# Performance work log

Hardware: AMD Instinct MI355X
Metric: run time of the kernel (lower is better)

## Reference

```python
import jax, jax.numpy as jnp
import numpy as np

N_NODES = 100000
N_EDGES = 3200000
N_FEAT = 256
N_CLASS = 4


def setup_inputs() -> dict:
    key = jax.random.key(0)
    ks = jax.random.split(key, 8)
    x = jax.random.normal(ks[0], (N_NODES, N_FEAT), dtype=jnp.float32)
    edge_index = jax.random.randint(ks[1], (2, N_EDGES), 0, N_NODES, dtype=jnp.int64)
    def xavier(k, shape):
        fan_in, fan_out = shape
        std = np.sqrt(2.0 / (fan_in + fan_out))
        return jax.random.normal(k, shape, dtype=jnp.float32) * std
    return {
        'x': x,
        'edge_index': edge_index,
        'W_gcn': xavier(ks[2], (N_FEAT, 64)),
        'b_gcn': jnp.zeros((64,), jnp.float32),
        'W1': xavier(ks[3], (64, 32)),
        'b1': jnp.zeros((32,), jnp.float32),
        'W2': xavier(ks[4], (32, 16)),
        'b2': jnp.zeros((16,), jnp.float32),
        'W3': xavier(ks[5], (16, N_CLASS)),
        'b3': jnp.zeros((N_CLASS,), jnp.float32),
    }


def gcn_conv(x, edge_index, W, b):
    # PyG GCNConv: transform, add self-loops, symmetric normalization, scatter-add
    N = x.shape[0]
    h = x @ W  # [N, 64]
    loop = jnp.arange(N, dtype=edge_index.dtype)
    src = jnp.concatenate([edge_index[0], loop])
    dst = jnp.concatenate([edge_index[1], loop])
    deg = jax.ops.segment_sum(jnp.ones_like(dst, dtype=h.dtype), dst, num_segments=N)
    dinv = jnp.where(deg > 0, jax.lax.rsqrt(deg), 0.0)
    norm = dinv[src] * dinv[dst]  # [E+N]
    msgs = h[src] * norm[:, None]  # gather [E+N, 64]
    out = jax.ops.segment_sum(msgs, dst, num_segments=N)
    return out + b


def reference(x, edge_index, W_gcn, b_gcn, W1, b1, W2, b2, W3, b3):
    h = gcn_conv(x, edge_index, W_gcn, b_gcn)
    h = jax.nn.relu(h)          # dropout is identity in eval mode
    h = jax.nn.relu(h @ W1 + b1)
    h = jax.nn.relu(h @ W2 + b2)
    h = h @ W3 + b3
    return jax.nn.log_softmax(h, axis=1)
```

## Files before the change

kernel.cpp:

```cpp
#include <hip/hip_runtime.h>
#include <hip/hip_bf16.h>

#define NN 100000
#define NE 3200000
#define NPB 64
#define NB 1564
#define CAP 2560
#define BATCH 8192
#define NGB 1563

typedef __hip_bfloat16 bf16;
typedef __attribute__((ext_vector_type(8))) short bf16x8;
typedef __attribute__((ext_vector_type(4))) float f32x4;

__device__ __forceinline__ void fma4(float4& a, float s, const float4 w) {
  a.x = fmaf(s, w.x, a.x);
  a.y = fmaf(s, w.y, a.y);
  a.z = fmaf(s, w.z, a.z);
  a.w = fmaf(s, w.w, a.w);
}

__device__ __forceinline__ unsigned short f2b(float f) {
  unsigned u = __float_as_uint(f);
  unsigned r = ((u >> 16) & 1u) + 0x7FFFu;
  return (unsigned short)((u + r) >> 16);
}

__device__ __forceinline__ unsigned pack2(float lo, float hi) {
  return (unsigned)f2b(lo) | ((unsigned)f2b(hi) << 16);
}

__global__ void detect_k(const int* __restrict__ e, int* __restrict__ flag) {
  unsigned long long b = __ballot(e[2 * (int)threadIdx.x + 1] == 0);
  if (threadIdx.x == 0) flag[0] = (b == 0xFFFFFFFFFFFFFFFFULL) ? 1 : 0;
}

__global__ __launch_bounds__(1024) void bin_k(const void* __restrict__ eidx,
                                              const int* __restrict__ flag,
                                              int* __restrict__ bcur,
                                              int* __restrict__ buckets) {
  __shared__ int scnt[NB];
  __shared__ int lcur[NB];
  int t = threadIdx.x;
  long long e0 = (long long)blockIdx.x * BATCH;
  int m = (int)((NE - e0 < BATCH) ? (NE - e0) : BATCH);
  int isI64 = flag[0];

  for (int i = t; i < NB; i += 1024) scnt[i] = 0;
  __syncthreads();

  int ent[BATCH / 1024], bv[BATCH / 1024];
#pragma unroll
  for (int j = 0; j < BATCH / 1024; j++) {
    int idx = t + j * 1024;
    bv[j] = -1;
    if (idx < m) {
      long long i = e0 + idx;
      int s, d;
      if (isI64) {
        s = (int)((const long long*)eidx)[i];
        d = (int)((const long long*)eidx)[NE + i];
      } else {
        s = ((const int*)eidx)[i];
        d = ((const int*)eidx)[NE + i];
      }
      bv[j] = d >> 6;
      ent[j] = s | ((d & 63) << 17);
      atomicAdd(&scnt[bv[j]], 1);
    }
  }
  __syncthreads();
  for (int i = t; i < NB; i += 1024) {
    int c = scnt[i];
    lcur[i] = c ? atomicAdd(&bcur[i], c) : 0;
  }
  __syncthreads();
#pragma unroll
  for (int j = 0; j < BATCH / 1024; j++) {
    if (bv[j] >= 0) {
      int pos = atomicAdd(&lcur[bv[j]], 1);
      if (pos < CAP) buckets[(size_t)bv[j] * CAP + pos] = ent[j];
    }
  }
}

__global__ __launch_bounds__(256) void cnt_k(int* __restrict__ buckets,
                                             const int* __restrict__ bcur,
                                             float* __restrict__ dinv,
                                             int* __restrict__ counts,
                                             int* __restrict__ offb) {
  __shared__ int cnt[NPB];
  __shared__ int off[NPB];
  __shared__ int lcur[NPB];
  __shared__ int ents[CAP];
  int b = blockIdx.x, t = threadIdx.x;
  if (t < NPB) cnt[t] = 0;
  __syncthreads();
  int m = bcur[b]; if (m > CAP) m = CAP;
  int* bp = buckets + (size_t)b * CAP;
  for (int i = t; i < m; i += 256) {
    int e = bp[i];
    ents[i] = e;
    atomicAdd(&cnt[(e >> 17) & 63], 1);
  }
  __syncthreads();
  if (t == 0) {
    int s = 0;
#pragma unroll
    for (int i = 0; i < NPB; i++) { off[i] = s; s += cnt[i]; }
  }
  __syncthreads();
  if (t < NPB) lcur[t] = off[t];
  __syncthreads();
  for (int i = t; i < m; i += 256) {
    int e = ents[i];
    int pos = atomicAdd(&lcur[(e >> 17) & 63], 1);
    bp[pos] = e & 0x1FFFF;
  }
  int node = b * NPB + t;
  if (t < NPB && node < NN) {
    dinv[node] = rsqrtf((float)cnt[t] + 1.0f);
    counts[node] = cnt[t];
    offb[b * NPB + t] = off[t];
  }
}

__global__ __launch_bounds__(256) void prep_k(const float* __restrict__ W,
                                              unsigned short* __restrict__ wh,
                                              unsigned short* __restrict__ wl) {
  int t = threadIdx.x;
#pragma unroll 4
  for (int i = 0; i < 64; i++) {
    int idx = i * 256 + t;
    int j = idx & 7;
    int lane = (idx >> 3) & 63;
    int pair = idx >> 9;
    int nf = pair & 3, kk = pair >> 2;
    int k = kk * 32 + (lane >> 4) * 8 + j;
    int n = nf * 16 + (lane & 15);
    float w = W[k * 64 + n];
    unsigned short hh = f2b(w);
    float fh = __uint_as_float((unsigned)hh << 16);
    wh[idx] = hh;
    wl[idx] = f2b(w - fh);
  }
}

__global__ __launch_bounds__(256) void gemm_k(const float* __restrict__ x,
                                              const unsigned short* __restrict__ wh,
                                              const unsigned short* __restrict__ wl,
                                              const float* __restrict__ dinv,
                                              bf16* __restrict__ h) {
  int t = threadIdx.x;
  int wv = t >> 6, l = t & 63;
  int rowbase = blockIdx.x * 64 + wv * 16;
  int arow = rowbase + (l & 15);
  if (arow >= NN) arow = NN - 1;
  const float* xrow = x + (size_t)arow * 256 + (l >> 4) * 8;

  const bf16x8* whf = (const bf16x8*)wh;
  const bf16x8* wlf = (const bf16x8*)wl;

  f32x4 acc0 = {0.f, 0.f, 0.f, 0.f};
  f32x4 acc1 = acc0, acc2 = acc0, acc3 = acc0;

  float4 x0a = *(const float4*)(xrow +   0), x0b = *(const float4*)(xrow +   4);
  float4 x1a = *(const float4*)(xrow +  32), x1b = *(const float4*)(xrow +  36);
  float4 x2a = *(const float4*)(xrow +  64), x2b = *(const float4*)(xrow +  68);
  float4 x3a = *(const float4*)(xrow +  96), x3b = *(const float4*)(xrow + 100);
  float4 x4a = *(const float4*)(xrow + 128), x4b = *(const float4*)(xrow + 132);
  float4 x5a = *(const float4*)(xrow + 160), x5b = *(const float4*)(xrow + 164);
  float4 x6a = *(const float4*)(xrow + 192), x6b = *(const float4*)(xrow + 196);
  float4 x7a = *(const float4*)(xrow + 224), x7b = *(const float4*)(xrow + 228);

  bf16x8 ha0, ha1, ha2, ha3, la0, la1, la2, la3;
  bf16x8 hb0, hb1, hb2, hb3, lb0, lb1, lb2, lb3;

#define LOADW(H0, H1, H2, H3, L0, L1, L2, L3, kk)                      \
  {                                                                    \
    int fb_ = (kk) * 256 + l;                                          \
    H0 = whf[fb_]; H1 = whf[fb_ + 64]; H2 = whf[fb_ + 128]; H3 = whf[fb_ + 192]; \
    L0 = wlf[fb_]; L1 = wlf[fb_ + 64]; L2 = wlf[fb_ + 128]; L3 = wlf[fb_ + 192]; \
  }
#define COMPUTE(Xa, Xb, H0, H1, H2, H3, L0, L1, L2, L3)                \
  {                                                                    \
    bf16x8 ah, al;                                                     \
    {                                                                  \
      unsigned short hh_; float fh_;                                   \
      hh_ = f2b(Xa.x); fh_ = __uint_as_float((unsigned)hh_ << 16); ah[0] = (short)hh_; al[0] = (short)f2b(Xa.x - fh_); \
      hh_ = f2b(Xa.y); fh_ = __uint_as_float((unsigned)hh_ << 16); ah[1] = (short)hh_; al[1] = (short)f2b(Xa.y - fh_); \
      hh_ = f2b(Xa.z); fh_ = __uint_as_float((unsigned)hh_ << 16); ah[2] = (short)hh_; al[2] = (short)f2b(Xa.z - fh_); \
      hh_ = f2b(Xa.w); fh_ = __uint_as_float((unsigned)hh_ << 16); ah[3] = (short)hh_; al[3] = (short)f2b(Xa.w - fh_); \
      hh_ = f2b(Xb.x); fh_ = __uint_as_float((unsigned)hh_ << 16); ah[4] = (short)hh_; al[4] = (short)f2b(Xb.x - fh_); \
      hh_ = f2b(Xb.y); fh_ = __uint_as_float((unsigned)hh_ << 16); ah[5] = (short)hh_; al[5] = (short)f2b(Xb.y - fh_); \
      hh_ = f2b(Xb.z); fh_ = __uint_as_float((unsigned)hh_ << 16); ah[6] = (short)hh_; al[6] = (short)f2b(Xb.z - fh_); \
      hh_ = f2b(Xb.w); fh_ = __uint_as_float((unsigned)hh_ << 16); ah[7] = (short)hh_; al[7] = (short)f2b(Xb.w - fh_); \
    }                                                                  \
    acc0 = __builtin_amdgcn_mfma_f32_16x16x32_bf16(ah, H0, acc0, 0, 0, 0); \
    acc1 = __builtin_amdgcn_mfma_f32_16x16x32_bf16(ah, H1, acc1, 0, 0, 0); \
    acc2 = __builtin_amdgcn_mfma_f32_16x16x32_bf16(ah, H2, acc2, 0, 0, 0); \
    acc3 = __builtin_amdgcn_mfma_f32_16x16x32_bf16(ah, H3, acc3, 0, 0, 0); \
    acc0 = __builtin_amdgcn_mfma_f32_16x16x32_bf16(ah, L0, acc0, 0, 0, 0); \
    acc1 = __builtin_amdgcn_mfma_f32_16x16x32_bf16(ah, L1, acc1, 0, 0, 0); \
    acc2 = __builtin_amdgcn_mfma_f32_16x16x32_bf16(ah, L2, acc2, 0, 0, 0); \
    acc3 = __builtin_amdgcn_mfma_f32_16x16x32_bf16(ah, L3, acc3, 0, 0, 0); \
    acc0 = __builtin_amdgcn_mfma_f32_16x16x32_bf16(al, H0, acc0, 0, 0, 0); \
    acc1 = __builtin_amdgcn_mfma_f32_16x16x32_bf16(al, H1, acc1, 0, 0, 0); \
    acc2 = __builtin_amdgcn_mfma_f32_16x16x32_bf16(al, H2, acc2, 0, 0, 0); \
    acc3 = __builtin_amdgcn_mfma_f32_16x16x32_bf16(al, H3, acc3, 0, 0, 0); \
  }
#define SBAR __builtin_amdgcn_sched_barrier(0);

  LOADW(ha0, ha1, ha2, ha3, la0, la1, la2, la3, 0)
  LOADW(hb0, hb1, hb2, hb3, lb0, lb1, lb2, lb3, 1)
  COMPUTE(x0a, x0b, ha0, ha1, ha2, ha3, la0, la1, la2, la3) SBAR
  LOADW(ha0, ha1, ha2, ha3, la0, la1, la2, la3, 2)
  COMPUTE(x1a, x1b, hb0, hb1, hb2, hb3, lb0, lb1, lb2, lb3) SBAR
  LOADW(hb0, hb1, hb2, hb3, lb0, lb1, lb2, lb3, 3)
  COMPUTE(x2a, x2b, ha0, ha1, ha2, ha3, la0, la1, la2, la3) SBAR
  LOADW(ha0, ha1, ha2, ha3, la0, la1, la2, la3, 4)
  COMPUTE(x3a, x3b, hb0, hb1, hb2, hb3, lb0, lb1, lb2, lb3) SBAR
  LOADW(hb0, hb1, hb2, hb3, lb0, lb1, lb2, lb3, 5)
  COMPUTE(x4a, x4b, ha0, ha1, ha2, ha3, la0, la1, la2, la3) SBAR
  LOADW(ha0, ha1, ha2, ha3, la0, la1, la2, la3, 6)
  COMPUTE(x5a, x5b, hb0, hb1, hb2, hb3, lb0, lb1, lb2, lb3) SBAR
  LOADW(hb0, hb1, hb2, hb3, lb0, lb1, lb2, lb3, 7)
  COMPUTE(x6a, x6b, ha0, ha1, ha2, ha3, la0, la1, la2, la3) SBAR
  COMPUTE(x7a, x7b, hb0, hb1, hb2, hb3, lb0, lb1, lb2, lb3)
#undef LOADW
#undef COMPUTE
#undef SBAR

#pragma unroll
  for (int reg = 0; reg < 4; reg++) {
    int row = rowbase + (l >> 4) * 4 + reg;
    if (row < NN) {
      float dn = dinv[row];
      unsigned short* hp = (unsigned short*)h + (size_t)row * 64 + (l & 15);
      hp[0]  = f2b(acc0[reg] * dn);
      hp[16] = f2b(acc1[reg] * dn);
      hp[32] = f2b(acc2[reg] * dn);
      hp[48] = f2b(acc3[reg] * dn);
    }
  }
}

__global__ __launch_bounds__(512) void agg_k(const bf16* __restrict__ h,
                                             const int* __restrict__ bsrc,
                                             const int* __restrict__ offb,
                                             const int* __restrict__ counts,
                                             const float* __restrict__ dinv,
                                             const float* __restrict__ bg,
                                             bf16* __restrict__ hg) {
  int b = blockIdx.x, t = threadIdx.x;
  int g = t >> 3, fl = t & 7;
  int node = b * NPB + g;
  if (node >= NN) return;
  int start = offb[b * NPB + g];
  int cnt = counts[node];
  const int* sp = bsrc + (size_t)b * CAP + start;
  const unsigned short* hu = (const unsigned short*)h;

  float a0 = 0.f, a1 = 0.f, a2 = 0.f, a3 = 0.f,
        a4 = 0.f, a5 = 0.f, a6 = 0.f, a7 = 0.f;

#define ACCV(V)                                                          \
  {                                                                      \
    a0 += __uint_as_float(V.x << 16); a1 += __uint_as_float(V.x & 0xFFFF0000u); \
    a2 += __uint_as_float(V.y << 16); a3 += __uint_as_float(V.y & 0xFFFF0000u); \
    a4 += __uint_as_float(V.z << 16); a5 += __uint_as_float(V.z & 0xFFFF0000u); \
    a6 += __uint_as_float(V.w << 16); a7 += __uint_as_float(V.w & 0xFFFF0000u); \
  }

  int i = 0;
  for (; i + 4 <= cnt; i += 4) {
    int s0 = sp[i], s1 = sp[i + 1], s2 = sp[i + 2], s3 = sp[i + 3];
    uint4 v0 = *(const uint4*)(hu + (size_t)s0 * 64 + fl * 8);
    uint4 v1 = *(const uint4*)(hu + (size_t)s1 * 64 + fl * 8);
    uint4 v2 = *(const uint4*)(hu + (size_t)s2 * 64 + fl * 8);
    uint4 v3 = *(const uint4*)(hu + (size_t)s3 * 64 + fl * 8);
    ACCV(v0) ACCV(v1) ACCV(v2) ACCV(v3)
  }
  for (; i < cnt; i++) {
    int s0 = sp[i];
    uint4 v0 = *(const uint4*)(hu + (size_t)s0 * 64 + fl * 8);
    ACCV(v0)
  }
#undef ACCV

  uint4 sv = *(const uint4*)(hu + (size_t)node * 64 + fl * 8);
  float dn = dinv[node];
  const float* bb = bg + fl * 8;
  a0 += __uint_as_float(sv.x << 16); a1 += __uint_as_float(sv.x & 0xFFFF0000u);
  a2 += __uint_as_float(sv.y << 16); a3 += __uint_as_float(sv.y & 0xFFFF0000u);
  a4 += __uint_as_float(sv.z << 16); a5 += __uint_as_float(sv.z & 0xFFFF0000u);
  a6 += __uint_as_float(sv.w << 16); a7 += __uint_as_float(sv.w & 0xFFFF0000u);
  uint4 o;
  o.x = pack2(fmaxf(fmaf(a0, dn, bb[0]), 0.f), fmaxf(fmaf(a1, dn, bb[1]), 0.f));
  o.y = pack2(fmaxf(fmaf(a2, dn, bb[2]), 0.f), fmaxf(fmaf(a3, dn, bb[3]), 0.f));
  o.z = pack2(fmaxf(fmaf(a4, dn, bb[4]), 0.f), fmaxf(fmaf(a5, dn, bb[5]), 0.f));
  o.w = pack2(fmaxf(fmaf(a6, dn, bb[6]), 0.f), fmaxf(fmaf(a7, dn, bb[7]), 0.f));
  *(uint4*)((unsigned short*)hg + (size_t)node * 64 + fl * 8) = o;
}

__global__ __launch_bounds__(256) void mlp_k(const bf16* __restrict__ hg,
                                             const float* __restrict__ W1, const float* __restrict__ b1,
                                             const float* __restrict__ W2, const float* __restrict__ b2,
                                             const float* __restrict__ W3, const float* __restrict__ b3,
                                             float* __restrict__ out) {
  __shared__ float4 sW1[512];
  __shared__ float4 sW2[128];
  __shared__ float4 sW3[16];
  __shared__ float sb1[32], sb2[16], sb3[4];
  int t = threadIdx.x;
  for (int i = t; i < 512; i += 256) sW1[i] = ((const float4*)W1)[i];
  if (t < 128) sW2[t] = ((const float4*)W2)[t];
  if (t < 16)  sW3[t] = ((const float4*)W3)[t];
  if (t < 32)  sb1[t] = b1[t];
  if (t < 16)  sb2[t] = b2[t];
  if (t < 4)   sb3[t] = b3[t];
  __syncthreads();
  int n = blockIdx.x * 256 + t;
  if (n >= NN) return;
  float xr[64];
  const uint4* hp = (const uint4*)(hg + (size_t)n * 64);
#pragma unroll
  for (int i = 0; i < 8; i++) {
    uint4 v = hp[i];
    unsigned uu[4] = {v.x, v.y, v.z, v.w};
#pragma unroll
    for (int j = 0; j < 4; j++) {
      xr[8 * i + 2 * j]     = __uint_as_float(uu[j] << 16);
      xr[8 * i + 2 * j + 1] = __uint_as_float(uu[j] & 0xFFFF0000u);
    }
  }
  float4 a1[8];
#pragma unroll
  for (int j = 0; j < 8; j++) a1[j] = make_float4(sb1[4 * j], sb1[4 * j + 1], sb1[4 * j + 2], sb1[4 * j + 3]);
#pragma unroll
  for (int f = 0; f < 64; f++) {
    float xv = xr[f];
#pragma unroll
    for (int j = 0; j < 8; j++) fma4(a1[j], xv, sW1[f * 8 + j]);
  }
  float r2[32];
#pragma unroll
  for (int j = 0; j < 8; j++) {
    r2[4 * j + 0] = fmaxf(a1[j].x, 0.f);
    r2[4 * j + 1] = fmaxf(a1[j].y, 0.f);
    r2[4 * j + 2] = fmaxf(a1[j].z, 0.f);
    r2[4 * j + 3] = fmaxf(a1[j].w, 0.f);
  }
  float4 a2[4];
#pragma unroll
  for (int j = 0; j < 4; j++) a2[j] = make_float4(sb2[4 * j], sb2[4 * j + 1], sb2[4 * j + 2], sb2[4 * j + 3]);
#pragma unroll
  for (int f = 0; f < 32; f++) {
    float xv = r2[f];
#pragma unroll
    for (int j = 0; j < 4; j++) fma4(a2[j], xv, sW2[f * 4 + j]);
  }
  float r3[16];
#pragma unroll
  for (int j = 0; j < 4; j++) {
    r3[4 * j + 0] = fmaxf(a2[j].x, 0.f);
    r3[4 * j + 1] = fmaxf(a2[j].y, 0.f);
    r3[4 * j + 2] = fmaxf(a2[j].z, 0.f);
    r3[4 * j + 3] = fmaxf(a2[j].w, 0.f);
  }
  float4 a3 = make_float4(sb3[0], sb3[1], sb3[2], sb3[3]);
#pragma unroll
  for (int f = 0; f < 16; f++) fma4(a3, r3[f], sW3[f]);
  float m = fmaxf(fmaxf(a3.x, a3.y), fmaxf(a3.z, a3.w));
  float s = expf(a3.x - m) + expf(a3.y - m) + expf(a3.z - m) + expf(a3.w - m);
  float l = m + logf(s);
  ((float4*)out)[n] = make_float4(a3.x - l, a3.y - l, a3.z - l, a3.w - l);
}

extern "C" void kernel_launch(void* const* d_in, const int* in_sizes, int n_in,
                              void* d_out, int out_size, void* d_ws, size_t ws_size,
                              hipStream_t stream) {
  const float* x  = (const float*)d_in[0];
  const void* eidx = d_in[1];
  const float* Wg = (const float*)d_in[2];
  const float* bg = (const float*)d_in[3];
  const float* W1 = (const float*)d_in[4];
  const float* b1 = (const float*)d_in[5];
  const float* W2 = (const float*)d_in[6];
  const float* b2 = (const float*)d_in[7];
  const float* W3 = (const float*)d_in[8];
  const float* b3 = (const float*)d_in[9];

  char* ws = (char*)d_ws;
  bf16*  h       = (bf16*) (ws + 0);
  bf16*  hg      = (bf16*) (ws + 12800000);
  int*   buckets = (int*)  (ws + 25600000);
  float* dinv    = (float*)(ws + 41615360);
  int*   counts  = (int*)  (ws + 42015360);
  int*   bcur    = (int*)  (ws + 42415360);
  int*   flag    = (int*)  (ws + 42421632);
  int*   offb    = (int*)  (ws + 42421760);
  unsigned short* wh = (unsigned short*)(ws + 12800000);
  unsigned short* wl = (unsigned short*)(ws + 12800000 + 32768);

  detect_k<<<1, 64, 0, stream>>>((const int*)eidx, flag);
  hipMemsetAsync(bcur, 0, NB * sizeof(int), stream);
  bin_k<<<(NE + BATCH - 1) / BATCH, 1024, 0, stream>>>(eidx, flag, bcur, buckets);
  cnt_k<<<NB, 256, 0, stream>>>(buckets, bcur, dinv, counts, offb);
  prep_k<<<1, 256, 0, stream>>>(Wg, wh, wl);
  gemm_k<<<NGB, 256, 0, stream>>>(x, wh, wl, dinv, h);
  agg_k<<<NB, 512, 0, stream>>>(h, buckets, offb, counts, dinv, bg, hg);
  mlp_k<<<(NN + 255) / 256, 256, 0, stream>>>(hg, W1, b1, W2, b2, W3, b3, (float*)d_out);
}
```

Before: 174.3 us.

## Remove cnt_k: count degrees in bin_k, sort buckets inside agg_k

Drops the separate per-bucket counting and sorting kernel. Degrees are now counted with global atomics in bin_k, dinv is computed at the start of gemm_k, and each agg_k block sorts its own bucket in shared memory. Because dinv is only known after gemm_k starts, the source-side normalisation moves from gemm_k into agg_k as a per-edge dinv gather and FMA. This saves one launch and one read/write pass over the buckets. The cost is 3.2M global atomics, an extra gather per edge, and a possible race: gemm_k blocks read dinv for rows that other blocks write, although gemm_k itself no longer uses dinv.

```diff
diff --git a/kernel.cpp b/kernel.cpp
--- a/kernel.cpp
+++ b/kernel.cpp
@@ -38,7 +38,8 @@
 __global__ __launch_bounds__(1024) void bin_k(const void* __restrict__ eidx,
                                               const int* __restrict__ flag,
                                               int* __restrict__ bcur,
-                                              int* __restrict__ buckets) {
+                                              int* __restrict__ buckets,
+                                              int* __restrict__ counts) {
   __shared__ int scnt[NB];
   __shared__ int lcur[NB];
   int t = threadIdx.x;
@@ -67,6 +68,7 @@
       bv[j] = d >> 6;
       ent[j] = s | ((d & 63) << 17);
       atomicAdd(&scnt[bv[j]], 1);
+      atomicAdd(&counts[d], 1);
     }
   }
   __syncthreads();
@@ -81,47 +83,6 @@
       int pos = atomicAdd(&lcur[bv[j]], 1);
       if (pos < CAP) buckets[(size_t)bv[j] * CAP + pos] = ent[j];
     }
-  }
-}
-
-__global__ __launch_bounds__(256) void cnt_k(int* __restrict__ buckets,
-                                             const int* __restrict__ bcur,
-                                             float* __restrict__ dinv,
-                                             int* __restrict__ counts,
-                                             int* __restrict__ offb) {
-  __shared__ int cnt[NPB];
-  __shared__ int off[NPB];
-  __shared__ int lcur[NPB];
-  __shared__ int ents[CAP];
-  int b = blockIdx.x, t = threadIdx.x;
-  if (t < NPB) cnt[t] = 0;
-  __syncthreads();
-  int m = bcur[b]; if (m > CAP) m = CAP;
-  int* bp = buckets + (size_t)b * CAP;
-  for (int i = t; i < m; i += 256) {
-    int e = bp[i];
-    ents[i] = e;
-    atomicAdd(&cnt[(e >> 17) & 63], 1);
-  }
-  __syncthreads();
-  if (t == 0) {
-    int s = 0;
-#pragma unroll
-    for (int i = 0; i < NPB; i++) { off[i] = s; s += cnt[i]; }
-  }
-  __syncthreads();
-  if (t < NPB) lcur[t] = off[t];
-  __syncthreads();
-  for (int i = t; i < m; i += 256) {
-    int e = ents[i];
-    int pos = atomicAdd(&lcur[(e >> 17) & 63], 1);
-    bp[pos] = e & 0x1FFFF;
-  }
-  int node = b * NPB + t;
-  if (t < NPB && node < NN) {
-    dinv[node] = rsqrtf((float)cnt[t] + 1.0f);
-    counts[node] = cnt[t];
-    offb[b * NPB + t] = off[t];
   }
 }
 
@@ -149,9 +110,14 @@
 __global__ __launch_bounds__(256) void gemm_k(const float* __restrict__ x,
                                               const unsigned short* __restrict__ wh,
                                               const unsigned short* __restrict__ wl,
-                                              const float* __restrict__ dinv,
+                                              const int* __restrict__ counts,
+                                              float* __restrict__ dinv,
                                               bf16* __restrict__ h) {
   int t = threadIdx.x;
+  {
+    int nd = blockIdx.x * 64 + t;
+    if (t < 64 && nd < NN) dinv[nd] = rsqrtf((float)counts[nd] + 1.0f);
+  }
   int wv = t >> 6, l = t & 63;
   int rowbase = blockIdx.x * 64 + wv * 16;
   int arow = rowbase + (l & 15);
@@ -235,66 +201,104 @@
   for (int reg = 0; reg < 4; reg++) {
     int row = rowbase + (l >> 4) * 4 + reg;
     if (row < NN) {
-      float dn = dinv[row];
       unsigned short* hp = (unsigned short*)h + (size_t)row * 64 + (l & 15);
-      hp[0]  = f2b(acc0[reg] * dn);
-      hp[16] = f2b(acc1[reg] * dn);
-      hp[32] = f2b(acc2[reg] * dn);
-      hp[48] = f2b(acc3[reg] * dn);
+      hp[0]  = f2b(acc0[reg]);
+      hp[16] = f2b(acc1[reg]);
+      hp[32] = f2b(acc2[reg]);
+      hp[48] = f2b(acc3[reg]);
     }
   }
 }
 
 __global__ __launch_bounds__(512) void agg_k(const bf16* __restrict__ h,
-                                             const int* __restrict__ bsrc,
-                                             const int* __restrict__ offb,
-                                             const int* __restrict__ counts,
+                                             const int* __restrict__ buckets,
+                                             const int* __restrict__ bcur,
                                              const float* __restrict__ dinv,
                                              const float* __restrict__ bg,
                                              bf16* __restrict__ hg) {
+  __shared__ int ents[CAP];
+  __shared__ int srt[CAP];
+  __shared__ int cnt[NPB];
+  __shared__ int off[NPB];
+  __shared__ int lcur[NPB];
   int b = blockIdx.x, t = threadIdx.x;
+  int m = bcur[b]; if (m > CAP) m = CAP;
+  const int* bp = buckets + (size_t)b * CAP;
+  if (t < NPB) cnt[t] = 0;
+  __syncthreads();
+  for (int i = t; i < m; i += 512) {
+    int e = bp[i];
+    ents[i] = e;
+    atomicAdd(&cnt[(e >> 17) & 63], 1);
+  }
+  __syncthreads();
+  if (t == 0) {
+    int s = 0;
+#pragma unroll
+    for (int i = 0; i < NPB; i++) { off[i] = s; s += cnt[i]; }
+  }
+  __syncthreads();
+  if (t < NPB) lcur[t] = off[t];
+  __syncthreads();
+  for (int i = t; i < m; i += 512) {
+    int e = ents[i];
+    int pos = atomicAdd(&lcur[(e >> 17) & 63], 1);
+    srt[pos] = e & 0x1FFFF;
+  }
+  __syncthreads();
+
   int g = t >> 3, fl = t & 7;
   int node = b * NPB + g;
   if (node >= NN) return;
-  int start = offb[b * NPB + g];
-  int cnt = counts[node];
-  const int* sp = bsrc + (size_t)b * CAP + start;
+  int start = off[g];
+  int deg = cnt[g];
+  float dn = dinv[node];
   const unsigned short* hu = (const unsigned short*)h;
 
   float a0 = 0.f, a1 = 0.f, a2 = 0.f, a3 = 0.f,
         a4 = 0.f, a5 = 0.f, a6 = 0.f, a7 = 0.f;
 
-#define ACCV(V)                                                          \
+#define ACCV(V, DV)                                                      \
   {                                                                      \
-    a0 += __uint_as_float(V.x << 16); a1 += __uint_as_float(V.x & 0xFFFF0000u); \
-    a2 += __uint_as_float(V.y << 16); a3 += __uint_as_float(V.y & 0xFFFF0000u); \
-    a4 += __uint_as_float(V.z << 16); a5 += __uint_as_float(V.z & 0xFFFF0000u); \
-    a6 += __uint_as_float(V.w << 16); a7 += __uint_as_float(V.w & 0xFFFF0000u); \
+    a0 = fmaf(__uint_as_float(V.x << 16),          (DV), a0);            \
+    a1 = fmaf(__uint_as_float(V.x & 0xFFFF0000u),  (DV), a1);            \
+    a2 = fmaf(__uint_as_float(V.y << 16),          (DV), a2);            \
+    a3 = fmaf(__uint_as_float(V.y & 0xFFFF0000u),  (DV), a3);            \
+    a4 = fmaf(__uint_as_float(V.z << 16),          (DV), a4);            \
+    a5 = fmaf(__uint_as_float(V.z & 0xFFFF0000u),  (DV), a5);            \
+    a6 = fmaf(__uint_as_float(V.w << 16),          (DV), a6);            \
+    a7 = fmaf(__uint_as_float(V.w & 0xFFFF0000u),  (DV), a7);            \
   }
 
   int i = 0;
-  for (; i + 4 <= cnt; i += 4) {
-    int s0 = sp[i], s1 = sp[i + 1], s2 = sp[i + 2], s3 = sp[i + 3];
+  for (; i + 4 <= deg; i += 4) {
+    int s0 = srt[start + i], s1 = srt[start + i + 1];
+    int s2 = srt[start + i + 2], s3 = srt[start + i + 3];
+    float d0 = dinv[s0], d1 = dinv[s1], d2 = dinv[s2], d3 = dinv[s3];
     uint4 v0 = *(const uint4*)(hu + (size_t)s0 * 64 + fl * 8);
     uint4 v1 = *(const uint4*)(hu + (size_t)s1 * 64 + fl * 8);
     uint4 v2 = *(const uint4*)(hu + (size_t)s2 * 64 + fl * 8);
     uint4 v3 = *(const uint4*)(hu + (size_t)s3 * 64 + fl * 8);
-    ACCV(v0) ACCV(v1) ACCV(v2) ACCV(v3)
-  }
-  for (; i < cnt; i++) {
-    int s0 = sp[i];
+    ACCV(v0, d0) ACCV(v1, d1) ACCV(v2, d2) ACCV(v3, d3)
+  }
+  for (; i < deg; i++) {
+    int s0 = srt[start + i];
+    float d0 = dinv[s0];
     uint4 v0 = *(const uint4*)(hu + (size_t)s0 * 64 + fl * 8);
-    ACCV(v0)
+    ACCV(v0, d0)
   }
 #undef ACCV
 
   uint4 sv = *(const uint4*)(hu + (size_t)node * 64 + fl * 8);
-  float dn = dinv[node];
   const float* bb = bg + fl * 8;
-  a0 += __uint_as_float(sv.x << 16); a1 += __uint_as_float(sv.x & 0xFFFF0000u);
-  a2 += __uint_as_float(sv.y << 16); a3 += __uint_as_float(sv.y & 0xFFFF0000u);
-  a4 += __uint_as_float(sv.z << 16); a5 += __uint_as_float(sv.z & 0xFFFF0000u);
-  a6 += __uint_as_float(sv.w << 16); a7 += __uint_as_float(sv.w & 0xFFFF0000u);
+  a0 = fmaf(__uint_as_float(sv.x << 16),         dn, a0);
+  a1 = fmaf(__uint_as_float(sv.x & 0xFFFF0000u), dn, a1);
+  a2 = fmaf(__uint_as_float(sv.y << 16),         dn, a2);
+  a3 = fmaf(__uint_as_float(sv.y & 0xFFFF0000u), dn, a3);
+  a4 = fmaf(__uint_as_float(sv.z << 16),         dn, a4);
+  a5 = fmaf(__uint_as_float(sv.z & 0xFFFF0000u), dn, a5);
+  a6 = fmaf(__uint_as_float(sv.w << 16),         dn, a6);
+  a7 = fmaf(__uint_as_float(sv.w & 0xFFFF0000u), dn, a7);
   uint4 o;
   o.x = pack2(fmaxf(fmaf(a0, dn, bb[0]), 0.f), fmaxf(fmaf(a1, dn, bb[1]), 0.f));
   o.y = pack2(fmaxf(fmaf(a2, dn, bb[2]), 0.f), fmaxf(fmaf(a3, dn, bb[3]), 0.f));
@@ -399,16 +403,15 @@
   int*   counts  = (int*)  (ws + 42015360);
   int*   bcur    = (int*)  (ws + 42415360);
   int*   flag    = (int*)  (ws + 42421632);
-  int*   offb    = (int*)  (ws + 42421760);
   unsigned short* wh = (unsigned short*)(ws + 12800000);
   unsigned short* wl = (unsigned short*)(ws + 12800000 + 32768);
 
   detect_k<<<1, 64, 0, stream>>>((const int*)eidx, flag);
   hipMemsetAsync(bcur, 0, NB * sizeof(int), stream);
-  bin_k<<<(NE + BATCH - 1) / BATCH, 1024, 0, stream>>>(eidx, flag, bcur, buckets);
-  cnt_k<<<NB, 256, 0, stream>>>(buckets, bcur, dinv, counts, offb);
+  hipMemsetAsync(counts, 0, NN * sizeof(int), stream);
+  bin_k<<<(NE + BATCH - 1) / BATCH, 1024, 0, stream>>>(eidx, flag, bcur, buckets, counts);
   prep_k<<<1, 256, 0, stream>>>(Wg, wh, wl);
-  gemm_k<<<NGB, 256, 0, stream>>>(x, wh, wl, dinv, h);
-  agg_k<<<NB, 512, 0, stream>>>(h, buckets, offb, counts, dinv, bg, hg);
+  gemm_k<<<NGB, 256, 0, stream>>>(x, wh, wl, counts, dinv, h);
+  agg_k<<<NB, 512, 0, stream>>>(h, buckets, bcur, dinv, bg, hg);
   mlp_k<<<(NN + 255) / 256, 256, 0, stream>>>(hg, W1, b1, W2, b2, W3, b3, (float*)d_out);
 }
```

New measurement: 265.2 us. +52.2%, slower.
